# Kernel tuning notes

Hardware: AMD Instinct MI355X
Metric: run time of the kernel (lower is better)

Reference implementation:

```python
import jax, jax.numpy as jnp
import numpy as np

B, N, K, H = 32, 1024, 10, 64  # graphs, nodes per graph, kNN, hidden_channels


def setup_inputs() -> dict:
    key = jax.random.key(0)
    ks = jax.random.split(key, 11)
    def w(k, shape, fan_in):
        lim = 1.0 / np.sqrt(fan_in)
        return jax.random.uniform(k, shape, jnp.float32, -lim, lim)
    return {
        'pos': jax.random.uniform(ks[0], (B, N, 2), jnp.float32),  # TSP city coords
        'W1': w(ks[1], (4, H), 4),           'b1': w(ks[2], (H,), 4),
        'W2': w(ks[3], (2 * H, 2 * H), 2 * H), 'b2': w(ks[4], (2 * H,), 2 * H),
        'W3': w(ks[5], (4 * H, 4 * H), 4 * H), 'b3': w(ks[6], (4 * H,), 4 * H),
        'Wl1': w(ks[7], (4 * H, H), 4 * H),   'bl1': w(ks[8], (H,), 4 * H),
        'Wl2': w(ks[9], (H, 2), H),           'bl2': w(ks[10], (2,), H),
    }


def _edge_conv(x, W, b, k):
    # DynamicEdgeConv: kNN graph in feature space (self-match included, as in
    # torch_cluster.knn(x, x, k)), edge feature [x_i, x_j - x_i], Linear, max-aggr.
    sq = jnp.sum(x * x, axis=-1)                                   # [B,N]
    dist = sq[:, :, None] + sq[:, None, :] - 2.0 * jnp.einsum('bnd,bmd->bnm', x, x)
    _, idx = jax.lax.top_k(-dist, k)                               # [B,N,k]
    xj = jax.vmap(lambda xb, ib: xb[ib])(x, idx)                   # [B,N,k,D]
    xi = x[:, :, None, :]
    edge = jnp.concatenate([jnp.broadcast_to(xi, xj.shape), xj - xi], axis=-1)
    msg = edge @ W + b                                             # [B,N,k,Dout]
    return jnp.max(msg, axis=2)                                    # max aggregation


def _pair_norm(x, eps=1e-5, scale=1.0):
    # PairNorm over all nodes (module calls it without batch vector)
    xc = x - jnp.mean(x, axis=(0, 1), keepdims=True)
    msn = jnp.mean(jnp.sum(xc * xc, axis=-1))  # mean squared node norm
    return scale * xc / jnp.sqrt(eps + msn)


def reference(pos, W1, b1, W2, b2, W3, b3, Wl1, bl1, Wl2, bl2):
    h1 = _pair_norm(jax.nn.relu(_edge_conv(pos, W1, b1, K)))
    h2 = _pair_norm(jax.nn.relu(_edge_conv(h1, W2, b2, K)))
    h3 = _pair_norm(jax.nn.relu(_edge_conv(h2, W3, b3, K)))
    g = jnp.max(h3, axis=1)                    # global_max_pool per graph -> [B,4H]
    h = jax.nn.relu(g @ Wl1 + bl1)             # dropout(p=0.2) is identity in eval
    return h @ Wl2 + bl2                       # [B,2]
```

## Files before the change

### kernel.cpp

```cpp
#include <hip/hip_runtime.h>
#include <math.h>

constexpr int NB = 32;
constexpr int NP = 1024;
constexpr int NK = 10;
constexpr int BN = NB * NP;
constexpr int NT = NP/128;
constexpr int NSLOT = 1024;

__device__ __forceinline__ float4 ld4(const float* p){ return *reinterpret_cast<const float4*>(p); }
__device__ __forceinline__ float2 ld2(const float* p){ return *reinterpret_cast<const float2*>(p); }
__device__ __forceinline__ void st4(float* p, float4 v){ *reinterpret_cast<float4*>(p) = v; }

__global__ __launch_bounds__(256) void k_sq_pos(const float* __restrict__ x, float* __restrict__ sq){
  int i = blockIdx.x*256 + threadIdx.x;
  float2 v = ld2(x + (size_t)2*i);
  sq[i] = v.x*v.x + v.y*v.y;
}

template<int DIN, int DOUT>
__global__ void k_wt(const float* __restrict__ W, float* __restrict__ WT){
  int n = blockIdx.x, k = threadIdx.x;
  float v = (n < DOUT) ? W[(size_t)k*DOUT + n]
                       : W[(size_t)DIN*DOUT + (size_t)k*DOUT + (n - DOUT)];
  WT[(size_t)n*DIN + k] = v;
}

__device__ __forceinline__ void sel_rows(float (&d)[8][8], int rx, int m0, float2* c0){
  float kv[8]; int kc[8];
#pragma unroll
  for (int k=0;k<8;++k){ kv[k] = 0.f; kc[k] = 0; }
#pragma unroll 1
  for (int sel=0; sel<NK; ++sel){
    float v[8]; int c[8];
#pragma unroll
    for (int k=0;k<8;++k){
      v[k] = d[k][0]; c[k] = rx*8;
#pragma unroll
      for (int l=1;l<8;++l){
        int cc = rx*8+l;
        if (d[k][l] < v[k]){ v[k] = d[k][l]; c[k] = cc; }
      }
    }
#pragma unroll
    for (int off=1; off<16; off<<=1){
#pragma unroll
      for (int k=0;k<8;++k){
        float ov = __shfl_xor(v[k], off, 64);
        int   oc = __shfl_xor(c[k], off, 64);
        if (ov < v[k] || (ov == v[k] && oc < c[k])){ v[k] = ov; c[k] = oc; }
      }
    }
#pragma unroll
    for (int k=0;k<8;++k){
      if (rx == (c[k]>>3)){
#pragma unroll
        for (int l=0;l<8;++l) if (l == (c[k]&7)) d[k][l] = __builtin_inff();
      }
    }
    if (rx == sel){
#pragma unroll
      for (int k=0;k<8;++k){ kv[k] = v[k]; kc[k] = c[k]; }
    }
  }
  if (rx < NK){
#pragma unroll
    for (int k=0;k<8;++k)
      c0[(size_t)k*(NT*NK) + rx] = make_float2(kv[k], (float)(m0 + kc[k]));
  }
}

__global__ __launch_bounds__(256) void k_knn2(const float* __restrict__ x,
    const float* __restrict__ sq, float2* __restrict__ cand){
  int b = blockIdx.z;
  int n0 = blockIdx.x*128, m0 = blockIdx.y*128;
  int ry = threadIdx.x>>4, rx = threadIdx.x&15;
  const float* xb = x + (size_t)b*NP*2;
  const float* sqb = sq + (size_t)b*NP;
  float2 av[8], bv[8]; float sn[8], sm[8];
#pragma unroll
  for (int k=0;k<8;++k){
    av[k] = ld2(xb + (size_t)(n0+ry*8+k)*2);
    bv[k] = ld2(xb + (size_t)(m0+rx*8+k)*2);
    sn[k] = sqb[n0+ry*8+k];
    sm[k] = sqb[m0+rx*8+k];
  }
  float d[8][8];
#pragma unroll
  for (int k=0;k<8;++k)
#pragma unroll
    for (int l=0;l<8;++l){
      float dot = av[k].x*bv[l].x + av[k].y*bv[l].y;
      d[k][l] = (sn[k] + sm[l]) - 2.f*dot;
    }
  sel_rows(d, rx, m0, cand + (((size_t)b*NP + n0 + ry*8)*NT + blockIdx.y)*NK);
}

template<int DIN>
__global__ __launch_bounds__(256) void k_knn(const float* __restrict__ x,
    const float* __restrict__ sq, float2* __restrict__ cand){
  constexpr int K4 = DIN/4, K4p = 8, NPH = K4/K4p, MASK = K4p-1;
  extern __shared__ float4 smem[];
  float4* as4 = smem;
  float4* bs4 = smem + 128*K4p;
  int b = blockIdx.z;
  int n0 = blockIdx.x*128, m0 = blockIdx.y*128;
  int ry = threadIdx.x>>4, rx = threadIdx.x&15;
  const float* xb = x + (size_t)b*NP*DIN;
  float acc[8][8];
#pragma unroll
  for (int k=0;k<8;++k)
#pragma unroll
    for (int l=0;l<8;++l) acc[k][l] = 0.f;
#pragma unroll 1
  for (int ph=0; ph<NPH; ++ph){
    __syncthreads();
    for (int u=threadIdx.x; u<128*K4p; u+=256){
      int r = u >> 3, c = u & 7;
      int sw = r*K4p + ((c + (r>>3)) & MASK);
      as4[sw] = ld4(xb + (size_t)(n0+r)*DIN + 4*(ph*K4p + c));
      bs4[sw] = ld4(xb + (size_t)(m0+r)*DIN + 4*(ph*K4p + c));
    }
    __syncthreads();
#pragma unroll 2
    for (int d4=0; d4<K4p; ++d4){
      float4 a_[8], b_[8];
#pragma unroll
      for (int k=0;k<8;++k) a_[k] = as4[(ry*8+k)*K4p + ((d4 + ry) & MASK)];
#pragma unroll
      for (int l=0;l<8;++l) b_[l] = bs4[(rx*8+l)*K4p + ((d4 + rx) & MASK)];
#pragma unroll
      for (int k=0;k<8;++k)
#pragma unroll
        for (int l=0;l<8;++l)
          acc[k][l] += a_[k].x*b_[l].x + a_[k].y*b_[l].y + a_[k].z*b_[l].z + a_[k].w*b_[l].w;
    }
  }
  const float* sqb = sq + (size_t)b*NP;
  float sn[8], sm[8];
#pragma unroll
  for (int k=0;k<8;++k){ sn[k] = sqb[n0+ry*8+k]; sm[k] = sqb[m0+rx*8+k]; }
#pragma unroll
  for (int k=0;k<8;++k)
#pragma unroll
    for (int l=0;l<8;++l) acc[k][l] = (sn[k]+sm[l]) - 2.f*acc[k][l];
  sel_rows(acc, rx, m0, cand + (((size_t)b*NP + n0 + ry*8)*NT + blockIdx.y)*NK);
}

__global__ __launch_bounds__(256) void k_merge(const float2* __restrict__ cand,
    int* __restrict__ idx){
  int wid = threadIdx.x>>6, lane = threadIdx.x&63;
  int row = blockIdx.x*4 + wid;
  const float2* cr = cand + (size_t)row*(NT*NK);
  float2 e0 = cr[lane];
  float v0 = e0.x; int c0 = (int)e0.y;
  float v1; int c1;
  if (lane < NT*NK - 64){ float2 e1 = cr[64+lane]; v1 = e1.x; c1 = (int)e1.y; }
  else { v1 = __builtin_inff(); c1 = 0x7fffffff; }
  int* out = idx + (size_t)row*NK;
  for (int sel=0; sel<NK; ++sel){
    float v; int c;
    if (v1 < v0 || (v1 == v0 && c1 < c0)){ v = v1; c = c1; } else { v = v0; c = c0; }
#pragma unroll
    for (int off=1; off<64; off<<=1){
      float ov = __shfl_xor(v, off, 64);
      int   oc = __shfl_xor(c, off, 64);
      if (ov < v || (ov == v && oc < c)){ v = ov; c = oc; }
    }
    if (c0 == c) v0 = __builtin_inff();
    if (c1 == c) v1 = __builtin_inff();
    if (lane == 0) out[sel] = c;
  }
}

template<int DIN, int DOUT>
__global__ __launch_bounds__(256) void k_gemm(const float* __restrict__ x,
    const float* __restrict__ WT, float* __restrict__ xcat, int m_base){
  constexpr int K4 = DIN/4, K4p = 8, NPH = K4/K4p, MASK = K4p-1;
  extern __shared__ float4 smem[];
  float4* as4 = smem;
  float4* bs4 = smem + 128*K4p;
  int m0 = blockIdx.x*128;
  int nc = blockIdx.y*128;
  const float* xg = x + (size_t)(m_base + m0)*DIN;
  const float* Bg = WT + (size_t)nc*DIN;
  int ry = threadIdx.x>>4, rx = threadIdx.x&15;
  float acc[8][8];
#pragma unroll
  for (int k=0;k<8;++k)
#pragma unroll
    for (int l=0;l<8;++l) acc[k][l] = 0.f;
#pragma unroll 1
  for (int ph=0; ph<NPH; ++ph){
    __syncthreads();
    for (int u=threadIdx.x; u<128*K4p; u+=256){
      int r = u >> 3, c = u & 7;
      int sw = r*K4p + ((c + (r>>3)) & MASK);
      as4[sw] = ld4(xg + (size_t)r*DIN + 4*(ph*K4p + c));
      bs4[sw] = ld4(Bg + (size_t)r*DIN + 4*(ph*K4p + c));
    }
    __syncthreads();
#pragma unroll 2
    for (int d4=0; d4<K4p; ++d4){
      float4 a_[8], b_[8];
#pragma unroll
      for (int k=0;k<8;++k) a_[k] = as4[(ry*8+k)*K4p + ((d4 + ry) & MASK)];
#pragma unroll
      for (int l=0;l<8;++l) b_[l] = bs4[(rx*8+l)*K4p + ((d4 + rx) & MASK)];
#pragma unroll
      for (int k=0;k<8;++k)
#pragma unroll
        for (int l=0;l<8;++l)
          acc[k][l] += a_[k].x*b_[l].x + a_[k].y*b_[l].y + a_[k].z*b_[l].z + a_[k].w*b_[l].w;
    }
  }
  float* outb = xcat + (size_t)(m0 + ry*8)*(2*DOUT) + nc + rx*8;
#pragma unroll
  for (int k=0;k<8;++k){
    st4(outb + (size_t)k*(2*DOUT),     make_float4(acc[k][0],acc[k][1],acc[k][2],acc[k][3]));
    st4(outb + (size_t)k*(2*DOUT) + 4, make_float4(acc[k][4],acc[k][5],acc[k][6],acc[k][7]));
  }
}

template<int DOUT>
__global__ __launch_bounds__(256) void k_gmax(const float* __restrict__ xcat,
    const int* __restrict__ idx, const float* __restrict__ bias,
    float* __restrict__ hout, float* __restrict__ spart, int p_base, int slot_base){
  constexpr int TP = DOUT/4;
  constexpr int ROWS = 256/TP;
  constexpr int PPT = 32/ROWS;
  __shared__ int idx_s[32*NK];
  __shared__ float red[1024];
  __shared__ float ssp[4];
  int c4 = threadIdx.x % TP, pr = threadIdx.x / TP;
  int c = 4*c4;
  int p0 = blockIdx.x*32 + p_base;
  for (int t=threadIdx.x; t<32*NK; t+=256) idx_s[t] = idx[(size_t)p0*NK + t];
  __syncthreads();
  float4 b4 = ld4(bias + c);
  float4 fsum = make_float4(0.f,0.f,0.f,0.f);
  float ss = 0.f;
  int pbl = (((p0 - p_base) >> 10) << 10);
#pragma unroll
  for (int t=0; t<PPT; ++t){
    int pl = pr + t*ROWS;
    int lrow = (p0 - p_base) + pl;
    const float* row = xcat + (size_t)lrow*(2*DOUT);
    float4 z = ld4(row + c), ys = ld4(row + DOUT + c);
    float4 mv = make_float4(-__builtin_inff(),-__builtin_inff(),-__builtin_inff(),-__builtin_inff());
    for (int j=0;j<NK;++j){
      int q = pbl + idx_s[pl*NK + j];
      float4 g = ld4(xcat + (size_t)q*(2*DOUT) + DOUT + c);
      mv.x = fmaxf(mv.x, g.x); mv.y = fmaxf(mv.y, g.y);
      mv.z = fmaxf(mv.z, g.z); mv.w = fmaxf(mv.w, g.w);
    }
    float4 v;
    v.x = fmaxf(z.x + b4.x - ys.x + mv.x, 0.f);
    v.y = fmaxf(z.y + b4.y - ys.y + mv.y, 0.f);
    v.z = fmaxf(z.z + b4.z - ys.z + mv.z, 0.f);
    v.w = fmaxf(z.w + b4.w - ys.w + mv.w, 0.f);
    st4(hout + (size_t)(p0 + pl)*DOUT + c, v);
    fsum.x += v.x; fsum.y += v.y; fsum.z += v.z; fsum.w += v.w;
    ss += v.x*v.x + v.y*v.y + v.z*v.z + v.w*v.w;
  }
  st4(&red[pr*DOUT + c], fsum);
#pragma unroll
  for (int off=32; off; off>>=1) ss += __shfl_xor(ss, off, 64);
  if ((threadIdx.x&63)==0) ssp[threadIdx.x>>6] = ss;
  __syncthreads();
  int slot = slot_base + blockIdx.x;
  for (int o=threadIdx.x; o<DOUT; o+=256){
    float s = 0.f;
#pragma unroll
    for (int r=0;r<ROWS;++r) s += red[r*DOUT + o];
    spart[(size_t)o*NSLOT + slot] = s;
  }
  if (threadIdx.x==0) spart[(size_t)DOUT*NSLOT + slot] = ssp[0]+ssp[1]+ssp[2]+ssp[3];
}

__global__ __launch_bounds__(256) void k_edge1(const float* __restrict__ x,
    const int* __restrict__ idx, const float* __restrict__ W,
    const float* __restrict__ bias, float* __restrict__ hout,
    float* __restrict__ spart){
  __shared__ int idx_s[32*NK];
  __shared__ float red[4][64];
  __shared__ float ssw[4];
  int lane = threadIdx.x & 63, wv = threadIdx.x >> 6;
  int p0 = blockIdx.x * 32;
  int b = p0 >> 10;
  int pl0 = p0 & 1023;
  const float* xb = x + ((size_t)b<<10)*2;
  for (int t=threadIdx.x; t<32*NK; t+=256) idx_s[t] = idx[(size_t)p0*NK + t];
  __syncthreads();
  float w0=W[lane], w1=W[64+lane], w2=W[128+lane], w3=W[192+lane];
  float bi = bias[lane];
  float fsum = 0.f, ss = 0.f;
#pragma unroll
  for (int t=0;t<8;++t){
    int pl = wv*8 + t;
    float2 xi = ld2(xb + (size_t)(pl0+pl)*2);
    float common = xi.x*w0 + xi.y*w1 + bi;
    float mv = -__builtin_inff();
    for (int j=0;j<NK;++j){
      float2 xj = ld2(xb + (size_t)idx_s[pl*NK+j]*2);
      mv = fmaxf(mv, (xj.x-xi.x)*w2 + (xj.y-xi.y)*w3);
    }
    float v = fmaxf(common + mv, 0.f);
    hout[(size_t)(p0+pl)*64 + lane] = v;
    fsum += v; ss += v*v;
  }
  red[wv][lane] = fsum;
#pragma unroll
  for (int off=32; off; off>>=1) ss += __shfl_xor(ss, off, 64);
  if (lane==0) ssw[wv] = ss;
  __syncthreads();
  if (threadIdx.x < 64){
    float s = red[0][lane]+red[1][lane]+red[2][lane]+red[3][lane];
    spart[(size_t)lane*NSLOT + blockIdx.x] = s;
  }
  if (threadIdx.x==0) spart[(size_t)64*NSLOT + blockIdx.x] = ssw[0]+ssw[1]+ssw[2]+ssw[3];
}

template<int DOUT>
__global__ __launch_bounds__(256) void k_finalize2(const float* __restrict__ spart,
    float* __restrict__ stats){
  __shared__ float part[4];
  __shared__ float ssh;
  float musq = 0.f;
  for (int f = threadIdx.x; f <= DOUT; f += 256){
    const float* row = spart + (size_t)f*NSLOT;
    float4 a = make_float4(0.f,0.f,0.f,0.f);
    for (int s=0; s<NSLOT; s+=4){
      float4 v = ld4(row + s);
      a.x += v.x; a.y += v.y; a.z += v.z; a.w += v.w;
    }
    float s = (a.x + a.y) + (a.z + a.w);
    if (f < DOUT){
      float m = s * (1.f/BN);
      stats[320+f] = m;
      musq += m*m;
    } else {
      ssh = s;
    }
  }
#pragma unroll
  for (int off=32; off; off>>=1) musq += __shfl_xor(musq, off, 64);
  if ((threadIdx.x&63)==0) part[threadIdx.x>>6] = musq;
  __syncthreads();
  if (threadIdx.x==0){
    float mu2 = part[0]+part[1]+part[2]+part[3];
    float msn = ssh*(1.f/BN) - mu2;
    stats[576] = 1.f / sqrtf(1e-5f + msn);
  }
}

template<int DOUT>
__global__ __launch_bounds__(256) void k_norm(float* __restrict__ h,
    const float* __restrict__ stats, float* __restrict__ sq){
  int lane = threadIdx.x&63, wv = threadIdx.x>>6;
  int row = blockIdx.x*4 + wv;
  float inv = stats[576];
  const float* mu = stats + 320;
  float* hr = h + (size_t)row*DOUT;
  float s = 0.f;
  if constexpr (DOUT == 64){
    float v = (hr[lane] - mu[lane]) * inv;
    hr[lane] = v;
    s = v*v;
  } else if constexpr (DOUT == 128){
    float2 x2 = ld2(hr + 2*lane), m2 = ld2(mu + 2*lane);
    float a = (x2.x - m2.x)*inv, b = (x2.y - m2.y)*inv;
    *reinterpret_cast<float2*>(hr + 2*lane) = make_float2(a,b);
    s = a*a + b*b;
  } else {
    float4 x4 = ld4(hr + 4*lane), m4 = ld4(mu + 4*lane);
    float4 v;
    v.x = (x4.x-m4.x)*inv; v.y = (x4.y-m4.y)*inv;
    v.z = (x4.z-m4.z)*inv; v.w = (x4.w-m4.w)*inv;
    st4(hr + 4*lane, v);
    s = v.x*v.x + v.y*v.y + v.z*v.z + v.w*v.w;
  }
#pragma unroll
  for (int off=32; off; off>>=1) s += __shfl_xor(s, off, 64);
  if (lane==0) sq[row] = s;
}

__global__ __launch_bounds__(256) void k_pool1(const float* __restrict__ h, float* __restrict__ gpart){
  int b = blockIdx.x, c = blockIdx.y, o = threadIdx.x;
  const float* hp = h + ((size_t)b*NP + c*128)*256 + o;
  float m = -__builtin_inff();
  for (int n=0;n<128;++n) m = fmaxf(m, hp[(size_t)n*256]);
  gpart[((size_t)c*NB + b)*256 + o] = m;
}

__global__ __launch_bounds__(256) void k_head(const float* __restrict__ gpart,
    const float* __restrict__ Wl1, const float* __restrict__ bl1,
    const float* __restrict__ Wl2, const float* __restrict__ bl2,
    float* __restrict__ out){
  __shared__ float g_s[256];
  __shared__ float h_s[64];
  int b = blockIdx.x, t = threadIdx.x;
  float m = -__builtin_inff();
  for (int c=0;c<8;++c) m = fmaxf(m, gpart[((size_t)c*NB + b)*256 + t]);
  g_s[t] = m;
  __syncthreads();
  if (t < 64){
    float a = bl1[t];
    for (int k=0;k<256;++k) a += g_s[k]*Wl1[(size_t)k*64 + t];
    h_s[t] = fmaxf(a, 0.f);
  }
  __syncthreads();
  if (t < 2){
    float a = bl2[t];
    for (int i=0;i<64;++i) a += h_s[i]*Wl2[(size_t)i*2 + t];
    out[(size_t)b*2 + t] = a;
  }
}

extern "C" void kernel_launch(void* const* d_in, const int* in_sizes, int n_in,
                              void* d_out, int out_size, void* d_ws, size_t ws_size,
                              hipStream_t stream){
  (void)in_sizes; (void)n_in; (void)out_size; (void)ws_size;
  const float* pos = (const float*)d_in[0];
  const float* W1  = (const float*)d_in[1];
  const float* b1  = (const float*)d_in[2];
  const float* W2  = (const float*)d_in[3];
  const float* b2  = (const float*)d_in[4];
  const float* W3  = (const float*)d_in[5];
  const float* b3  = (const float*)d_in[6];
  const float* Wl1 = (const float*)d_in[7];
  const float* bl1 = (const float*)d_in[8];
  const float* Wl2 = (const float*)d_in[9];
  const float* bl2 = (const float*)d_in[10];
  float* outp = (float*)d_out;

  (void)hipFuncSetAttribute((const void*)k_knn<128>,       hipFuncAttributeMaxDynamicSharedMemorySize, 32768);
  (void)hipFuncSetAttribute((const void*)k_knn<64>,        hipFuncAttributeMaxDynamicSharedMemorySize, 32768);
  (void)hipFuncSetAttribute((const void*)k_gemm<128,256>,  hipFuncAttributeMaxDynamicSharedMemorySize, 32768);
  (void)hipFuncSetAttribute((const void*)k_gemm<64,128>,   hipFuncAttributeMaxDynamicSharedMemorySize, 32768);

  char* w = (char*)d_ws;
  size_t off = 0;
  auto take = [&](size_t bytes)->char*{ char* p = w + off; off += (bytes + 255) & ~(size_t)255; return p; };
  float* sq    = (float*)take((size_t)BN*4);
  int*   idx   = (int*)  take((size_t)BN*NK*4);
  float* x1    = (float*)take((size_t)BN*64*4);
  float* x2    = (float*)take((size_t)BN*128*4);
  float* x3    = (float*)take((size_t)BN*256*4);
  float* stats = (float*)take(4096);
  float* spart = (float*)take((size_t)257*NSLOT*4);
  float* gpart = (float*)take((size_t)8*NB*256*4);
  float* wt2   = (float*)take((size_t)256*64*4);
  float* wt3   = (float*)take((size_t)512*128*4);
  float* big   = (float*)take((size_t)BN*(2*256)*4);
  float2* cand = (float2*)big;
  float* xcat  = big;

  dim3 gknn(NP/128, NP/128, NB);

  k_wt<64,128><<<256, 64, 0, stream>>>(W2, wt2);
  k_wt<128,256><<<512, 128, 0, stream>>>(W3, wt3);

  k_sq_pos<<<BN/256, 256, 0, stream>>>(pos, sq);
  k_knn2<<<gknn, 256, 0, stream>>>(pos, sq, cand);
  k_merge<<<BN/4, 256, 0, stream>>>(cand, idx);
  k_edge1<<<NSLOT, 256, 0, stream>>>(pos, idx, W1, b1, x1, spart);
  k_finalize2<64><<<1, 256, 0, stream>>>(spart, stats);
  k_norm<64><<<BN/4, 256, 0, stream>>>(x1, stats, sq);

  k_knn<64><<<gknn, 256, 32768, stream>>>(x1, sq, cand);
  k_merge<<<BN/4, 256, 0, stream>>>(cand, idx);
  k_gemm<64,128><<<dim3(BN/128, 2), 256, 32768, stream>>>(x1, wt2, xcat, 0);
  k_gmax<128><<<BN/32, 256, 0, stream>>>(xcat, idx, b2, x2, spart, 0, 0);
  k_finalize2<128><<<1, 256, 0, stream>>>(spart, stats);
  k_norm<128><<<BN/4, 256, 0, stream>>>(x2, stats, sq);

  k_knn<128><<<gknn, 256, 32768, stream>>>(x2, sq, cand);
  k_merge<<<BN/4, 256, 0, stream>>>(cand, idx);
  for (int h=0; h<2; ++h){
    int m_base = h * (BN/2);
    k_gemm<128,256><<<dim3(BN/2/128, 4), 256, 32768, stream>>>(x2, wt3, xcat, m_base);
    k_gmax<256><<<BN/2/32, 256, 0, stream>>>(xcat, idx, b3, x3, spart, m_base, h*(BN/2/32));
  }
  k_finalize2<256><<<1, 256, 0, stream>>>(spart, stats);
  k_norm<256><<<BN/4, 256, 0, stream>>>(x3, stats, sq);

  k_pool1<<<dim3(NB, 8), 256, 0, stream>>>(x3, gpart);
  k_head<<<NB, 256, 0, stream>>>(gpart, Wl1, bl1, Wl2, bl2, outp);
}
```

Before: 959.1 us.

## Exploit distance symmetry in kNN by computing only upper-triangular tiles

The feature-space kNN kernels now launch 36 upper-triangular 128x128 tiles per graph instead of 64. Each off-diagonal tile does its usual row-wise top-k selection and then a second column-wise top-k pass, written through LDS, which produces the candidate list for the transposed tile. This removes almost half of the distance GEMM work. In exchange the off-diagonal tiles pay extra selection passes, shuffles, a serial 40-way merge run by only 128 threads, and get more register pressure. The grid is also smaller, which may lower occupancy.

```diff
diff --git a/kernel.cpp b/kernel.cpp
--- a/kernel.cpp
+++ b/kernel.cpp
@@ -26,8 +26,8 @@
   WT[(size_t)n*DIN + k] = v;
 }
 
-__device__ __forceinline__ void sel_rows(float (&d)[8][8], int rx, int m0, float2* c0){
-  float kv[8]; int kc[8];
+__device__ __forceinline__ void sel_rows(float (&d)[8][8], int rx, int m0, float2* c0,
+                                         float (&kv)[8], int (&kc)[8]){
 #pragma unroll
   for (int k=0;k<8;++k){ kv[k] = 0.f; kc[k] = 0; }
 #pragma unroll 1
@@ -93,7 +93,8 @@
       float dot = av[k].x*bv[l].x + av[k].y*bv[l].y;
       d[k][l] = (sn[k] + sm[l]) - 2.f*dot;
     }
-  sel_rows(d, rx, m0, cand + (((size_t)b*NP + n0 + ry*8)*NT + blockIdx.y)*NK);
+  float kv[8]; int kc[8];
+  sel_rows(d, rx, m0, cand + (((size_t)b*NP + n0 + ry*8)*NT + blockIdx.y)*NK, kv, kc);
 }
 
 template<int DIN>
@@ -103,8 +104,11 @@
   extern __shared__ float4 smem[];
   float4* as4 = smem;
   float4* bs4 = smem + 128*K4p;
+  int t = blockIdx.x, ti = 0;
+  while (t >= 8 - ti){ t -= 8 - ti; ++ti; }
+  int tj = ti + t;
   int b = blockIdx.z;
-  int n0 = blockIdx.x*128, m0 = blockIdx.y*128;
+  int n0 = ti*128, m0 = tj*128;
   int ry = threadIdx.x>>4, rx = threadIdx.x&15;
   const float* xb = x + (size_t)b*NP*DIN;
   float acc[8][8];
@@ -144,7 +148,83 @@
   for (int k=0;k<8;++k)
 #pragma unroll
     for (int l=0;l<8;++l) acc[k][l] = (sn[k]+sm[l]) - 2.f*acc[k][l];
-  sel_rows(acc, rx, m0, cand + (((size_t)b*NP + n0 + ry*8)*NT + blockIdx.y)*NK);
+
+  float kv[8]; int kc[8];
+  sel_rows(acc, rx, m0, cand + (((size_t)b*NP + n0 + ry*8)*NT + tj)*NK, kv, kc);
+
+  if (ti != tj){
+    int lid = threadIdx.x & 63;
+#pragma unroll
+    for (int s=0; s<NK; ++s){
+#pragma unroll
+      for (int k=0;k<8;++k){
+        float rv = __shfl(kv[k], (lid & 48) + s, 64);
+        int   rc = __shfl(kc[k], (lid & 48) + s, 64);
+        if (rx == (rc>>3)){
+#pragma unroll
+          for (int l=0;l<8;++l) if (l == (rc&7)) acc[k][l] = rv;
+        }
+      }
+    }
+    __syncthreads();
+    float* v_lds = (float*)smem;
+    unsigned char* n_lds = (unsigned char*)(v_lds + 128*43);
+    int w = threadIdx.x >> 6;
+    int RY = threadIdx.x >> 4;
+    int ry4 = RY & 3;
+#pragma unroll 1
+    for (int s=0; s<NK; ++s){
+      float v[8]; int cn[8];
+#pragma unroll
+      for (int l=0;l<8;++l){
+        v[l] = acc[0][l]; cn[l] = RY*8;
+#pragma unroll
+        for (int k=1;k<8;++k){
+          int cc = RY*8 + k;
+          if (acc[k][l] < v[l]){ v[l] = acc[k][l]; cn[l] = cc; }
+        }
+      }
+#pragma unroll
+      for (int off=16; off<64; off<<=1){
+#pragma unroll
+        for (int l=0;l<8;++l){
+          float ov = __shfl_xor(v[l], off, 64);
+          int   on = __shfl_xor(cn[l], off, 64);
+          if (ov < v[l] || (ov == v[l] && on < cn[l])){ v[l] = ov; cn[l] = on; }
+        }
+      }
+#pragma unroll
+      for (int l=0;l<8;++l){
+        if (RY == (cn[l]>>3)){
+          int kw = cn[l] & 7;
+#pragma unroll
+          for (int k=0;k<8;++k) if (k == kw) acc[k][l] = __builtin_inff();
+        }
+        if (ry4 == (s & 3)){
+          int col = rx*8 + l;
+          v_lds[col*43 + w*10 + s] = v[l];
+          n_lds[col*43 + w*10 + s] = (unsigned char)cn[l];
+        }
+      }
+    }
+    __syncthreads();
+    if (threadIdx.x < 128){
+      int col = threadIdx.x;
+      float2* outr = cand + (((size_t)b*NP + m0 + col)*NT + ti)*NK;
+#pragma unroll 1
+      for (int s=0; s<NK; ++s){
+        float bv = v_lds[col*43]; int bi = 0;
+#pragma unroll 1
+        for (int q=1; q<40; ++q){
+          float vv = v_lds[col*43 + q];
+          if (vv < bv){ bv = vv; bi = q; }
+        }
+        int nn = n_lds[col*43 + bi];
+        v_lds[col*43 + bi] = __builtin_inff();
+        outr[s] = make_float2(bv, (float)(n0 + nn));
+      }
+    }
+  }
 }
 
 __global__ __launch_bounds__(256) void k_merge(const float2* __restrict__ cand,
@@ -456,26 +536,27 @@
   float2* cand = (float2*)big;
   float* xcat  = big;
 
-  dim3 gknn(NP/128, NP/128, NB);
+  dim3 gknn2(NP/128, NP/128, NB);
+  dim3 gsym(36, 1, NB);
 
   k_wt<64,128><<<256, 64, 0, stream>>>(W2, wt2);
   k_wt<128,256><<<512, 128, 0, stream>>>(W3, wt3);
 
   k_sq_pos<<<BN/256, 256, 0, stream>>>(pos, sq);
-  k_knn2<<<gknn, 256, 0, stream>>>(pos, sq, cand);
+  k_knn2<<<gknn2, 256, 0, stream>>>(pos, sq, cand);
   k_merge<<<BN/4, 256, 0, stream>>>(cand, idx);
   k_edge1<<<NSLOT, 256, 0, stream>>>(pos, idx, W1, b1, x1, spart);
   k_finalize2<64><<<1, 256, 0, stream>>>(spart, stats);
   k_norm<64><<<BN/4, 256, 0, stream>>>(x1, stats, sq);
 
-  k_knn<64><<<gknn, 256, 32768, stream>>>(x1, sq, cand);
+  k_knn<64><<<gsym, 256, 32768, stream>>>(x1, sq, cand);
   k_merge<<<BN/4, 256, 0, stream>>>(cand, idx);
   k_gemm<64,128><<<dim3(BN/128, 2), 256, 32768, stream>>>(x1, wt2, xcat, 0);
   k_gmax<128><<<BN/32, 256, 0, stream>>>(xcat, idx, b2, x2, spart, 0, 0);
   k_finalize2<128><<<1, 256, 0, stream>>>(spart, stats);
   k_norm<128><<<BN/4, 256, 0, stream>>>(x2, stats, sq);
 
-  k_knn<128><<<gknn, 256, 32768, stream>>>(x2, sq, cand);
+  k_knn<128><<<gsym, 256, 32768, stream>>>(x2, sq, cand);
   k_merge<<<BN/4, 256, 0, stream>>>(cand, idx);
   for (int h=0; h<2; ++h){
     int m_base = h * (BN/2);
```

New measurement: 1.222 ms. 27.4% more time.

## Fuse kNN candidate merge into edge-conv gather kernels and drop sq_pos kernel

Applied to the files above, without the earlier changes.

Removes the standalone k_merge kernels by merging per-tile top-k candidates inside k_edge1 and k_gmax via a per-block merge_rows helper, and computes squared norms inline in k_knn2 instead of in a separate k_sq_pos kernel. The candidate buffer gets its own workspace allocation instead of aliasing xcat. This cuts kernel launches and the round trip of idx through global memory. In exchange the merge work sits on the critical path of the gather kernels, and each wave now handles 8 rows serially.

```diff
diff --git a/kernel.cpp b/kernel.cpp
--- a/kernel.cpp
+++ b/kernel.cpp
@@ -12,12 +12,6 @@
 __device__ __forceinline__ float2 ld2(const float* p){ return *reinterpret_cast<const float2*>(p); }
 __device__ __forceinline__ void st4(float* p, float4 v){ *reinterpret_cast<float4*>(p) = v; }
 
-__global__ __launch_bounds__(256) void k_sq_pos(const float* __restrict__ x, float* __restrict__ sq){
-  int i = blockIdx.x*256 + threadIdx.x;
-  float2 v = ld2(x + (size_t)2*i);
-  sq[i] = v.x*v.x + v.y*v.y;
-}
-
 template<int DIN, int DOUT>
 __global__ void k_wt(const float* __restrict__ W, float* __restrict__ WT){
   int n = blockIdx.x, k = threadIdx.x;
@@ -70,20 +64,48 @@
   }
 }
 
+__device__ __forceinline__ void merge_rows(const float2* __restrict__ cand,
+    size_t p0, int* idx_s){
+  int lane = threadIdx.x & 63, w = threadIdx.x >> 6;
+#pragma unroll 1
+  for (int t=0; t<8; ++t){
+    int pl = w*8 + t;
+    const float2* cr = cand + (p0 + pl)*(size_t)(NT*NK);
+    float2 e0 = cr[lane];
+    float v0 = e0.x; int c0 = (int)e0.y;
+    float v1; int c1;
+    if (lane < NT*NK - 64){ float2 e1 = cr[64+lane]; v1 = e1.x; c1 = (int)e1.y; }
+    else { v1 = __builtin_inff(); c1 = 0x7fffffff; }
+#pragma unroll 1
+    for (int sel=0; sel<NK; ++sel){
+      float v; int c;
+      if (v1 < v0 || (v1 == v0 && c1 < c0)){ v = v1; c = c1; } else { v = v0; c = c0; }
+#pragma unroll
+      for (int off=1; off<64; off<<=1){
+        float ov = __shfl_xor(v, off, 64);
+        int   oc = __shfl_xor(c, off, 64);
+        if (ov < v || (ov == v && oc < c)){ v = ov; c = oc; }
+      }
+      if (c0 == c) v0 = __builtin_inff();
+      if (c1 == c) v1 = __builtin_inff();
+      if (lane == 0) idx_s[pl*NK + sel] = c;
+    }
+  }
+}
+
 __global__ __launch_bounds__(256) void k_knn2(const float* __restrict__ x,
-    const float* __restrict__ sq, float2* __restrict__ cand){
+    float2* __restrict__ cand){
   int b = blockIdx.z;
   int n0 = blockIdx.x*128, m0 = blockIdx.y*128;
   int ry = threadIdx.x>>4, rx = threadIdx.x&15;
   const float* xb = x + (size_t)b*NP*2;
-  const float* sqb = sq + (size_t)b*NP;
   float2 av[8], bv[8]; float sn[8], sm[8];
 #pragma unroll
   for (int k=0;k<8;++k){
     av[k] = ld2(xb + (size_t)(n0+ry*8+k)*2);
     bv[k] = ld2(xb + (size_t)(m0+rx*8+k)*2);
-    sn[k] = sqb[n0+ry*8+k];
-    sm[k] = sqb[m0+rx*8+k];
+    sn[k] = av[k].x*av[k].x + av[k].y*av[k].y;
+    sm[k] = bv[k].x*bv[k].x + bv[k].y*bv[k].y;
   }
   float d[8][8];
 #pragma unroll
@@ -145,32 +167,6 @@
 #pragma unroll
     for (int l=0;l<8;++l) acc[k][l] = (sn[k]+sm[l]) - 2.f*acc[k][l];
   sel_rows(acc, rx, m0, cand + (((size_t)b*NP + n0 + ry*8)*NT + blockIdx.y)*NK);
-}
-
-__global__ __launch_bounds__(256) void k_merge(const float2* __restrict__ cand,
-    int* __restrict__ idx){
-  int wid = threadIdx.x>>6, lane = threadIdx.x&63;
-  int row = blockIdx.x*4 + wid;
-  const float2* cr = cand + (size_t)row*(NT*NK);
-  float2 e0 = cr[lane];
-  float v0 = e0.x; int c0 = (int)e0.y;
-  float v1; int c1;
-  if (lane < NT*NK - 64){ float2 e1 = cr[64+lane]; v1 = e1.x; c1 = (int)e1.y; }
-  else { v1 = __builtin_inff(); c1 = 0x7fffffff; }
-  int* out = idx + (size_t)row*NK;
-  for (int sel=0; sel<NK; ++sel){
-    float v; int c;
-    if (v1 < v0 || (v1 == v0 && c1 < c0)){ v = v1; c = c1; } else { v = v0; c = c0; }
-#pragma unroll
-    for (int off=1; off<64; off<<=1){
-      float ov = __shfl_xor(v, off, 64);
-      int   oc = __shfl_xor(c, off, 64);
-      if (ov < v || (ov == v && oc < c)){ v = ov; c = oc; }
-    }
-    if (c0 == c) v0 = __builtin_inff();
-    if (c1 == c) v1 = __builtin_inff();
-    if (lane == 0) out[sel] = c;
-  }
 }
 
 template<int DIN, int DOUT>
@@ -224,7 +220,7 @@
 
 template<int DOUT>
 __global__ __launch_bounds__(256) void k_gmax(const float* __restrict__ xcat,
-    const int* __restrict__ idx, const float* __restrict__ bias,
+    const float2* __restrict__ cand, const float* __restrict__ bias,
     float* __restrict__ hout, float* __restrict__ spart, int p_base, int slot_base){
   constexpr int TP = DOUT/4;
   constexpr int ROWS = 256/TP;
@@ -235,7 +231,7 @@
   int c4 = threadIdx.x % TP, pr = threadIdx.x / TP;
   int c = 4*c4;
   int p0 = blockIdx.x*32 + p_base;
-  for (int t=threadIdx.x; t<32*NK; t+=256) idx_s[t] = idx[(size_t)p0*NK + t];
+  merge_rows(cand, (size_t)p0, idx_s);
   __syncthreads();
   float4 b4 = ld4(bias + c);
   float4 fsum = make_float4(0.f,0.f,0.f,0.f);
@@ -279,7 +275,7 @@
 }
 
 __global__ __launch_bounds__(256) void k_edge1(const float* __restrict__ x,
-    const int* __restrict__ idx, const float* __restrict__ W,
+    const float2* __restrict__ cand, const float* __restrict__ W,
     const float* __restrict__ bias, float* __restrict__ hout,
     float* __restrict__ spart){
   __shared__ int idx_s[32*NK];
@@ -290,7 +286,7 @@
   int b = p0 >> 10;
   int pl0 = p0 & 1023;
   const float* xb = x + ((size_t)b<<10)*2;
-  for (int t=threadIdx.x; t<32*NK; t+=256) idx_s[t] = idx[(size_t)p0*NK + t];
+  merge_rows(cand, (size_t)p0, idx_s);
   __syncthreads();
   float w0=W[lane], w1=W[64+lane], w2=W[128+lane], w3=W[192+lane];
   float bi = bias[lane];
@@ -442,45 +438,39 @@
   char* w = (char*)d_ws;
   size_t off = 0;
   auto take = [&](size_t bytes)->char*{ char* p = w + off; off += (bytes + 255) & ~(size_t)255; return p; };
-  float* sq    = (float*)take((size_t)BN*4);
-  int*   idx   = (int*)  take((size_t)BN*NK*4);
-  float* x1    = (float*)take((size_t)BN*64*4);
-  float* x2    = (float*)take((size_t)BN*128*4);
-  float* x3    = (float*)take((size_t)BN*256*4);
-  float* stats = (float*)take(4096);
-  float* spart = (float*)take((size_t)257*NSLOT*4);
-  float* gpart = (float*)take((size_t)8*NB*256*4);
-  float* wt2   = (float*)take((size_t)256*64*4);
-  float* wt3   = (float*)take((size_t)512*128*4);
-  float* big   = (float*)take((size_t)BN*(2*256)*4);
-  float2* cand = (float2*)big;
-  float* xcat  = big;
+  float*  sq    = (float*)take((size_t)BN*4);
+  float*  x1    = (float*)take((size_t)BN*64*4);
+  float*  x2    = (float*)take((size_t)BN*128*4);
+  float*  x3    = (float*)take((size_t)BN*256*4);
+  float*  stats = (float*)take(4096);
+  float*  spart = (float*)take((size_t)257*NSLOT*4);
+  float*  gpart = (float*)take((size_t)8*NB*256*4);
+  float*  wt2   = (float*)take((size_t)256*64*4);
+  float*  wt3   = (float*)take((size_t)512*128*4);
+  float2* cand  = (float2*)take((size_t)BN*NT*NK*8);
+  float*  xcat  = (float*)take((size_t)BN*256*4);
 
   dim3 gknn(NP/128, NP/128, NB);
 
   k_wt<64,128><<<256, 64, 0, stream>>>(W2, wt2);
   k_wt<128,256><<<512, 128, 0, stream>>>(W3, wt3);
 
-  k_sq_pos<<<BN/256, 256, 0, stream>>>(pos, sq);
-  k_knn2<<<gknn, 256, 0, stream>>>(pos, sq, cand);
-  k_merge<<<BN/4, 256, 0, stream>>>(cand, idx);
-  k_edge1<<<NSLOT, 256, 0, stream>>>(pos, idx, W1, b1, x1, spart);
+  k_knn2<<<gknn, 256, 0, stream>>>(pos, cand);
+  k_edge1<<<BN/32, 256, 0, stream>>>(pos, cand, W1, b1, x1, spart);
   k_finalize2<64><<<1, 256, 0, stream>>>(spart, stats);
   k_norm<64><<<BN/4, 256, 0, stream>>>(x1, stats, sq);
 
   k_knn<64><<<gknn, 256, 32768, stream>>>(x1, sq, cand);
-  k_merge<<<BN/4, 256, 0, stream>>>(cand, idx);
   k_gemm<64,128><<<dim3(BN/128, 2), 256, 32768, stream>>>(x1, wt2, xcat, 0);
-  k_gmax<128><<<BN/32, 256, 0, stream>>>(xcat, idx, b2, x2, spart, 0, 0);
+  k_gmax<128><<<BN/32, 256, 0, stream>>>(xcat, cand, b2, x2, spart, 0, 0);
   k_finalize2<128><<<1, 256, 0, stream>>>(spart, stats);
   k_norm<128><<<BN/4, 256, 0, stream>>>(x2, stats, sq);
 
   k_knn<128><<<gknn, 256, 32768, stream>>>(x2, sq, cand);
-  k_merge<<<BN/4, 256, 0, stream>>>(cand, idx);
   for (int h=0; h<2; ++h){
     int m_base = h * (BN/2);
     k_gemm<128,256><<<dim3(BN/2/128, 4), 256, 32768, stream>>>(x2, wt3, xcat, m_base);
-    k_gmax<256><<<BN/2/32, 256, 0, stream>>>(xcat, idx, b3, x3, spart, m_base, h*(BN/2/32));
+    k_gmax<256><<<BN/2/32, 256, 0, stream>>>(xcat, cand, b3, x3, spart, m_base, h*(BN/2/32));
   }
   k_finalize2<256><<<1, 256, 0, stream>>>(spart, stats);
   k_norm<256><<<BN/4, 256, 0, stream>>>(x3, stats, sq);
```

Result: slower. 1.038 ms (+8.2%).
